# Optimization experiments

Hardware: AMD Instinct MI355X
Metric: run time of the kernel (lower is better)

Reference implementation:

```python
import jax, jax.numpy as jnp
import numpy as np

DILS = [2 ** i for i in range(9)] * 7  # 27 residual-only layers + 36 layers with skip
N0 = 27  # first 27 layers (dilations0) do not contribute to skip connections


def _dconv(x, w, b, d):
    # dilated 'same' conv1d: x [B,C,T], w [O,I,3]
    y = jax.lax.conv_general_dilated(x, w, (1,), [(d, d)], rhs_dilation=(d,),
                                     dimension_numbers=('NCH', 'OIH', 'NCH'))
    return y + b[None, :, None]


def _pw(x, w, b):
    # 1x1 conv: w [O,C], x [B,C,T]
    return jnp.einsum('oc,bct->bot', w, x) + b[None, :, None]


def setup_inputs() -> dict:
    key = jax.random.key(0)
    ks = jax.random.split(key, 13)
    B, T, rd, sd, qd, L = 8, 16384, 128, 128, 256, 63
    s = 0.05
    f = lambda k, sh: jax.random.normal(k, sh, jnp.float32) * s
    return {
        'x': jax.random.normal(ks[0], (B, 1, T), jnp.float32),
        'causal_w': f(ks[1], (rd, 1, 25)),
        'causal_b': f(ks[2], (rd,)),
        'dcnn_w': f(ks[3], (L, rd, rd, 3)),
        'dcnn_b': f(ks[4], (L, rd)),
        'dense_w': f(ks[5], (L, rd, rd)),
        'dense_b': f(ks[6], (L, rd)),
        'skip_w': f(ks[7], (L, sd, rd)),
        'skip_b': f(ks[8], (L, sd)),
        'post1_w': f(ks[9], (sd, sd)),
        'post1_b': f(ks[10], (sd,)),
        'post2_w': f(ks[11], (qd, sd)),
        'post2_b': f(ks[12], (qd,)),
    }


def reference(x, causal_w, causal_b, dcnn_w, dcnn_b, dense_w, dense_b,
              skip_w, skip_b, post1_w, post1_b, post2_w, post2_b):
    # causal conv: kernel 25, padding 12 ('same')
    x = jax.lax.conv_general_dilated(x, causal_w, (1,), [(12, 12)],
                                     dimension_numbers=('NCH', 'OIH', 'NCH'))
    x = x + causal_b[None, :, None]
    B, _, T = x.shape
    skip = jnp.zeros((B, skip_w.shape[1], T), x.dtype)
    for cnt, d in enumerate(DILS):
        xin = x
        h = jax.nn.relu(x)
        h = jax.nn.relu(_dconv(h, dcnn_w[cnt], dcnn_b[cnt], d))
        if cnt >= N0:
            skip = skip + _pw(h, skip_w[cnt], skip_b[cnt])
        x = _pw(h, dense_w[cnt], dense_b[cnt]) + xin
    h = jax.nn.relu(_pw(jax.nn.relu(skip), post1_w, post1_b))
    return _pw(h, post2_w, post2_b)
```

## Files before the change

### kernel.cpp

```cpp
#include <hip/hip_runtime.h>

#define RD     128
#define TT     128
#define TLEN   16384
#define NB     8
#define NLAYER 63
#define N0SKIP 27
#define QD     256
#define PADR   136
#define SROWS  192

typedef short bf16x8 __attribute__((ext_vector_type(8)));
typedef float f32x4  __attribute__((ext_vector_type(4)));

__device__ __forceinline__ unsigned short f2bf(float f) {
  unsigned u = __float_as_uint(f);
  u += 0x7fffu + ((u >> 16) & 1u);
  return (unsigned short)(u >> 16);
}
__device__ __forceinline__ short f2bf_relu(float f) {
  f = f > 0.f ? f : 0.f;
  unsigned u = __float_as_uint(f);
  u += 0x7fffu + ((u >> 16) & 1u);
  return (short)(u >> 16);
}

__device__ __forceinline__ void mfma_gemm(const unsigned short* __restrict__ aw,
                                          const short* sx, int rowbase,
                                          int c0w, int t0w, int n, int q,
                                          f32x4 (&acc)[4][4]) {
#pragma unroll
  for (int ks = 0; ks < 4; ++ks) {
    const int i0 = ks * 32 + q * 8;
    bf16x8 a[4], bb[4];
#pragma unroll
    for (int ct = 0; ct < 4; ++ct)
      a[ct] = *(const bf16x8*)&aw[(size_t)(c0w + ct * 16 + n) * RD + i0];
#pragma unroll
    for (int tt = 0; tt < 4; ++tt)
      bb[tt] = *(const bf16x8*)&sx[(rowbase + t0w + tt * 16 + n) * PADR + i0];
#pragma unroll
    for (int ct = 0; ct < 4; ++ct)
#pragma unroll
      for (int tt = 0; tt < 4; ++tt)
        acc[ct][tt] = __builtin_amdgcn_mfma_f32_16x16x32_bf16(a[ct], bb[tt],
                                                              acc[ct][tt], 0, 0, 0);
  }
}

__device__ __forceinline__ void zero_acc(f32x4 (&acc)[4][4]) {
#pragma unroll
  for (int i = 0; i < 4; ++i)
#pragma unroll
    for (int j = 0; j < 4; ++j) acc[i][j] = (f32x4){0.f, 0.f, 0.f, 0.f};
}

#define SUNROLL 8
__device__ __forceinline__ void stage_rows(short* sx, int rowbase,
                                           const float* __restrict__ xb,
                                           int tstart, int nrows, int tid) {
  const int total = nrows * 32;
  int idx = tid;
  for (; idx + 256 * (SUNROLL - 1) < total; idx += 256 * SUNROLL) {
    float4 v[SUNROLL];
#pragma unroll
    for (int u = 0; u < SUNROLL; ++u) {
      const int i2 = idx + u * 256;
      const int tg = tstart + (i2 >> 5);
      const int c4 = (i2 & 31) << 2;
      v[u] = make_float4(0.f, 0.f, 0.f, 0.f);
      if ((unsigned)tg < (unsigned)TLEN)
        v[u] = *(const float4*)&xb[(size_t)tg * RD + c4];
    }
#pragma unroll
    for (int u = 0; u < SUNROLL; ++u) {
      const int i2 = idx + u * 256;
      const int r = i2 >> 5;
      const int c4 = (i2 & 31) << 2;
      short4 o;
      o.x = f2bf_relu(v[u].x); o.y = f2bf_relu(v[u].y);
      o.z = f2bf_relu(v[u].z); o.w = f2bf_relu(v[u].w);
      *(short4*)&sx[(rowbase + r) * PADR + c4] = o;
    }
  }
  for (; idx < total; idx += 256) {
    const int tg = tstart + (idx >> 5);
    const int c4 = (idx & 31) << 2;
    float4 v = make_float4(0.f, 0.f, 0.f, 0.f);
    if ((unsigned)tg < (unsigned)TLEN)
      v = *(const float4*)&xb[(size_t)tg * RD + c4];
    short4 o;
    o.x = f2bf_relu(v.x); o.y = f2bf_relu(v.y);
    o.z = f2bf_relu(v.z); o.w = f2bf_relu(v.w);
    *(short4*)&sx[(rowbase + (idx >> 5)) * PADR + c4] = o;
  }
}

__device__ __forceinline__ void store_act_bf16(short* dst, const f32x4 (&acc)[4][4],
                                               const float* __restrict__ bias,
                                               int c0w, int t0w, int n, int q) {
#pragma unroll
  for (int ct = 0; ct < 4; ++ct) {
    const int c = c0w + ct * 16 + q * 4;
    const float4 bb = *(const float4*)&bias[c];
#pragma unroll
    for (int tt = 0; tt < 4; ++tt) {
      const int t = t0w + tt * 16 + n;
      const f32x4 A = acc[ct][tt];
      short4 o;
      o.x = f2bf_relu(A[0] + bb.x);
      o.y = f2bf_relu(A[1] + bb.y);
      o.z = f2bf_relu(A[2] + bb.z);
      o.w = f2bf_relu(A[3] + bb.w);
      *(short4*)&dst[t * PADR + c] = o;
    }
  }
}

__device__ __forceinline__ void epi_accum(float* __restrict__ dst,
                                          const float* __restrict__ src,
                                          const float* __restrict__ bias,
                                          const f32x4 (&acc)[4][4],
                                          int c0w, int t0w, int n, int q) {
#pragma unroll
  for (int ct = 0; ct < 4; ++ct) {
    const int c = c0w + ct * 16 + q * 4;
    const float4 bb = *(const float4*)&bias[c];
#pragma unroll
    for (int tt = 0; tt < 4; ++tt) {
      const int t = t0w + tt * 16 + n;
      float4 r = *(const float4*)&src[(size_t)t * RD + c];
      const f32x4 A = acc[ct][tt];
      r.x += A[0] + bb.x; r.y += A[1] + bb.y;
      r.z += A[2] + bb.z; r.w += A[3] + bb.w;
      *(float4*)&dst[(size_t)t * RD + c] = r;
    }
  }
}

__global__ __launch_bounds__(256, 2) void layer_kernel(
    const float* __restrict__ x_in, float* __restrict__ x_out,
    float* __restrict__ skip,
    const unsigned short* __restrict__ wconv,
    const float* __restrict__ bconv,
    const unsigned short* __restrict__ wdense, const float* __restrict__ bdense,
    const unsigned short* __restrict__ wskip,  const float* __restrict__ bskip,
    int dil, int do_skip) {
  __shared__ short sx[SROWS * PADR];

  const int tid = threadIdx.x;
  const int bid = blockIdx.x;
  const int swz = (bid & 7) * 128 + (bid >> 3);
  const int b   = swz >> 7;
  const int t0  = (swz & 127) << 7;
  const int lane = tid & 63;
  const int n = lane & 15, q = lane >> 4;
  const int w = tid >> 6;
  const int c0w = (w & 1) * 64, t0w = (w >> 1) * 64;
  const float* xb = x_in + (size_t)b * TLEN * RD;

  f32x4 acc[4][4];
  zero_acc(acc);

  if (dil <= 32) {
    stage_rows(sx, 0, xb, t0 - dil, 128 + 2 * dil, tid);
    __syncthreads();
    for (int k = 0; k < 3; ++k)
      mfma_gemm(wconv + (size_t)k * RD * RD, sx, k * dil, c0w, t0w, n, q, acc);
  } else if (dil == 64) {
    stage_rows(sx, 0, xb, t0 - 64, 192, tid);
    __syncthreads();
    mfma_gemm(wconv, sx, 0, c0w, t0w, n, q, acc);
    mfma_gemm(wconv + (size_t)RD * RD, sx, 64, c0w, t0w, n, q, acc);
    __syncthreads();
    stage_rows(sx, 0, xb, t0 + 128, 64, tid);
    __syncthreads();
    mfma_gemm(wconv + (size_t)2 * RD * RD, sx, (t0w == 0) ? 128 : -64,
              c0w, t0w, n, q, acc);
  } else {
#pragma unroll
    for (int k = 0; k < 3; ++k) {
      stage_rows(sx, 0, xb, t0 + (k - 1) * dil, 128, tid);
      __syncthreads();
      mfma_gemm(wconv + (size_t)k * RD * RD, sx, 0, c0w, t0w, n, q, acc);
      __syncthreads();
    }
  }
  __syncthreads();

  store_act_bf16(sx, acc, bconv, c0w, t0w, n, q);
  __syncthreads();

  zero_acc(acc);
  mfma_gemm(wdense, sx, 0, c0w, t0w, n, q, acc);
  {
    float* xo = x_out + ((size_t)b * TLEN + t0) * RD;
    const float* xi = x_in + ((size_t)b * TLEN + t0) * RD;
    epi_accum(xo, xi, bdense, acc, c0w, t0w, n, q);
  }

  if (do_skip) {
    zero_acc(acc);
    mfma_gemm(wskip, sx, 0, c0w, t0w, n, q, acc);
    float* sp = skip + ((size_t)b * TLEN + t0) * RD;
    epi_accum(sp, sp, bskip, acc, c0w, t0w, n, q);
  }
}

__global__ __launch_bounds__(256) void causal_kernel(const float* __restrict__ x,
                                                     const float* __restrict__ w,
                                                     const float* __restrict__ bias,
                                                     float* __restrict__ y) {
  __shared__ float xw[152];
  __shared__ float wl[RD * 25];
  __shared__ float bl[RD];
  const int tid = threadIdx.x;
  const int b   = blockIdx.x >> 7;
  const int t0  = (blockIdx.x & 127) << 7;
  for (int i = tid; i < RD * 25; i += 256) wl[i] = w[i];
  if (tid < RD) bl[tid] = bias[tid];
  for (int i = tid; i < 152; i += 256) {
    const int tg = t0 - 12 + i;
    xw[i] = ((unsigned)tg < (unsigned)TLEN) ? x[(size_t)b * TLEN + tg] : 0.f;
  }
  __syncthreads();
  const int c = tid & 127, tp = tid >> 7;
  float* yb = y + ((size_t)b * TLEN + t0) * RD + c;
  const float bc = bl[c];
  for (int i = 0; i < 64; ++i) {
    const int tl = i * 2 + tp;
    float s = bc;
#pragma unroll
    for (int k = 0; k < 25; ++k) s = fmaf(wl[c * 25 + k], xw[tl + k], s);
    yb[(size_t)tl * RD] = s;
  }
}

__global__ __launch_bounds__(256, 1) void post_kernel(
    const float* __restrict__ skip,
    const unsigned short* __restrict__ p1, const float* __restrict__ p1b,
    const unsigned short* __restrict__ p2, const float* __restrict__ p2b,
    float* __restrict__ out) {
  __shared__ short sb[128 * PADR];
  __shared__ short h1[128 * PADR];
  __shared__ float ost[128 * 132];

  const int tid = threadIdx.x;
  const int b   = blockIdx.x >> 7;
  const int t0  = (blockIdx.x & 127) << 7;
  const int lane = tid & 63;
  const int n = lane & 15, q = lane >> 4;
  const int w = tid >> 6;
  const int c0w = (w & 1) * 64, t0w = (w >> 1) * 64;
  const float* skb = skip + ((size_t)b * TLEN + t0) * RD;

  for (int idx = tid; idx < 128 * 32; idx += 256) {
    const int r = idx >> 5, c4 = (idx & 31) << 2;
    float4 v = *(const float4*)&skb[(size_t)r * RD + c4];
    short4 o;
    o.x = f2bf_relu(v.x); o.y = f2bf_relu(v.y);
    o.z = f2bf_relu(v.z); o.w = f2bf_relu(v.w);
    *(short4*)&sb[r * PADR + c4] = o;
  }
  __syncthreads();

  f32x4 acc[4][4];
  zero_acc(acc);
  mfma_gemm(p1, sb, 0, c0w, t0w, n, q, acc);
  store_act_bf16(h1, acc, p1b, c0w, t0w, n, q);
  __syncthreads();

  for (int half = 0; half < 2; ++half) {
    zero_acc(acc);
    mfma_gemm(p2 + (size_t)half * RD * RD, h1, 0, c0w, t0w, n, q, acc);
#pragma unroll
    for (int ct = 0; ct < 4; ++ct) {
      const int c = c0w + ct * 16 + q * 4;
      const float4 bb = *(const float4*)&p2b[half * RD + c];
#pragma unroll
      for (int tt = 0; tt < 4; ++tt) {
        const int t = t0w + tt * 16 + n;
        const f32x4 A = acc[ct][tt];
        ost[(c + 0) * 132 + t] = A[0] + bb.x;
        ost[(c + 1) * 132 + t] = A[1] + bb.y;
        ost[(c + 2) * 132 + t] = A[2] + bb.z;
        ost[(c + 3) * 132 + t] = A[3] + bb.w;
      }
    }
    __syncthreads();
    float* ob = out + ((size_t)b * QD + half * RD) * TLEN + t0;
    for (int idx = tid; idx < 128 * 32; idx += 256) {
      const int r = idx >> 5, t4 = (idx & 31) << 2;
      const float4 v = *(const float4*)&ost[r * 132 + t4];
      *(float4*)&ob[(size_t)r * TLEN + t4] = v;
    }
    __syncthreads();
  }
}

__global__ __launch_bounds__(256) void cvt_kernel(const float* __restrict__ in,
                                                  unsigned short* __restrict__ out,
                                                  int total) {
  const int i = blockIdx.x * 256 + threadIdx.x;
  if (i < total) out[i] = f2bf(in[i]);
}
__global__ __launch_bounds__(256) void cvt_conv_kernel(const float* __restrict__ in,
                                                       unsigned short* __restrict__ out,
                                                       int total) {
  const int idx = blockIdx.x * 256 + threadIdx.x;
  if (idx >= total) return;
  const int ci = idx & 127, co = (idx >> 7) & 127, lk = idx >> 14;
  const int k = lk % 3, l = lk / 3;
  out[idx] = f2bf(in[(((size_t)l * RD + co) * RD + ci) * 3 + k]);
}

extern "C" void kernel_launch(void* const* d_in, const int* in_sizes, int n_in,
                              void* d_out, int out_size, void* d_ws, size_t ws_size,
                              hipStream_t stream) {
  const float* x        = (const float*)d_in[0];
  const float* causal_w = (const float*)d_in[1];
  const float* causal_b = (const float*)d_in[2];
  const float* dcnn_w   = (const float*)d_in[3];
  const float* dcnn_b   = (const float*)d_in[4];
  const float* dense_w  = (const float*)d_in[5];
  const float* dense_b  = (const float*)d_in[6];
  const float* skip_w   = (const float*)d_in[7];
  const float* skip_b   = (const float*)d_in[8];
  const float* post1_w  = (const float*)d_in[9];
  const float* post1_b  = (const float*)d_in[10];
  const float* post2_w  = (const float*)d_in[11];
  const float* post2_b  = (const float*)d_in[12];
  float* out = (float*)d_out;

  const size_t XN = (size_t)NB * TLEN * RD;
  float* ws  = (float*)d_ws;
  float* xA  = ws;
  float* xB  = xA + XN;
  float* skp = xB + XN;
  unsigned short* wc  = (unsigned short*)(skp + XN);
  unsigned short* wd  = wc  + (size_t)NLAYER * 3 * RD * RD;
  unsigned short* wsk = wd  + (size_t)NLAYER * RD * RD;
  unsigned short* p1  = wsk + (size_t)NLAYER * RD * RD;
  unsigned short* p2  = p1  + RD * RD;

  const int tconv = NLAYER * 3 * RD * RD;
  const int t2    = NLAYER * RD * RD;
  cvt_conv_kernel<<<(tconv + 255) / 256, 256, 0, stream>>>(dcnn_w, wc, tconv);
  cvt_kernel<<<(t2 + 255) / 256, 256, 0, stream>>>(dense_w, wd, t2);
  cvt_kernel<<<(t2 + 255) / 256, 256, 0, stream>>>(skip_w, wsk, t2);
  cvt_kernel<<<(RD * RD + 255) / 256, 256, 0, stream>>>(post1_w, p1, RD * RD);
  cvt_kernel<<<(QD * RD + 255) / 256, 256, 0, stream>>>(post2_w, p2, QD * RD);

  causal_kernel<<<NB * (TLEN / TT), 256, 0, stream>>>(x, causal_w, causal_b, xA);
  hipMemsetAsync(skp, 0, XN * sizeof(float), stream);

  const float* src = xA;
  float* dst = xB;
  for (int l = 0; l < NLAYER; ++l) {
    const int dil = 1 << (l % 9);
    layer_kernel<<<NB * (TLEN / TT), 256, 0, stream>>>(
        src, dst, skp,
        wc  + (size_t)l * 3 * RD * RD, dcnn_b  + (size_t)l * RD,
        wd  + (size_t)l * RD * RD,     dense_b + (size_t)l * RD,
        wsk + (size_t)l * RD * RD,     skip_b  + (size_t)l * RD,
        dil, (l >= N0SKIP) ? 1 : 0);
    const float* tmp = src; src = dst; dst = (float*)tmp;
  }

  post_kernel<<<NB * (TLEN / TT), 256, 0, stream>>>(skp, p1, post1_b, p2, post2_b, out);
}
```

Before: 4.824 ms.

## Stage halo reads from a bf16 relu shadow copy and keep residual in place

Each layer now writes, alongside the fp32 residual, a bf16 copy of relu(x), and the next layer stages its dilated-conv input (including halo rows) from that half-size buffer instead of re-reading and converting fp32. The fp32 residual is updated in place in one buffer, and the residual and skip tiles are prefetched into registers before the GEMMs so their loads overlap compute. This trades an extra bf16 store per layer for halving the staging read traffic. It also raises register pressure with two 4x4 float4 tiles held per thread, under a launch bound of two blocks.

```diff
diff --git a/kernel.cpp b/kernel.cpp
--- a/kernel.cpp
+++ b/kernel.cpp
@@ -57,42 +57,32 @@
 
 #define SUNROLL 8
 __device__ __forceinline__ void stage_rows(short* sx, int rowbase,
-                                           const float* __restrict__ xb,
+                                           const unsigned short* __restrict__ shb,
                                            int tstart, int nrows, int tid) {
-  const int total = nrows * 32;
+  const int total = nrows * 16;
   int idx = tid;
   for (; idx + 256 * (SUNROLL - 1) < total; idx += 256 * SUNROLL) {
-    float4 v[SUNROLL];
+    bf16x8 v[SUNROLL];
 #pragma unroll
     for (int u = 0; u < SUNROLL; ++u) {
       const int i2 = idx + u * 256;
-      const int tg = tstart + (i2 >> 5);
-      const int c4 = (i2 & 31) << 2;
-      v[u] = make_float4(0.f, 0.f, 0.f, 0.f);
+      const int tg = tstart + (i2 >> 4);
+      v[u] = (bf16x8)(short)0;
       if ((unsigned)tg < (unsigned)TLEN)
-        v[u] = *(const float4*)&xb[(size_t)tg * RD + c4];
+        v[u] = *(const bf16x8*)&shb[(size_t)tg * RD + ((i2 & 15) << 3)];
     }
 #pragma unroll
     for (int u = 0; u < SUNROLL; ++u) {
       const int i2 = idx + u * 256;
-      const int r = i2 >> 5;
-      const int c4 = (i2 & 31) << 2;
-      short4 o;
-      o.x = f2bf_relu(v[u].x); o.y = f2bf_relu(v[u].y);
-      o.z = f2bf_relu(v[u].z); o.w = f2bf_relu(v[u].w);
-      *(short4*)&sx[(rowbase + r) * PADR + c4] = o;
+      *(bf16x8*)&sx[(rowbase + (i2 >> 4)) * PADR + ((i2 & 15) << 3)] = v[u];
     }
   }
   for (; idx < total; idx += 256) {
-    const int tg = tstart + (idx >> 5);
-    const int c4 = (idx & 31) << 2;
-    float4 v = make_float4(0.f, 0.f, 0.f, 0.f);
+    const int tg = tstart + (idx >> 4);
+    bf16x8 v = (bf16x8)(short)0;
     if ((unsigned)tg < (unsigned)TLEN)
-      v = *(const float4*)&xb[(size_t)tg * RD + c4];
-    short4 o;
-    o.x = f2bf_relu(v.x); o.y = f2bf_relu(v.y);
-    o.z = f2bf_relu(v.z); o.w = f2bf_relu(v.w);
-    *(short4*)&sx[(rowbase + (idx >> 5)) * PADR + c4] = o;
+      v = *(const bf16x8*)&shb[(size_t)tg * RD + ((idx & 15) << 3)];
+    *(bf16x8*)&sx[(rowbase + (idx >> 4)) * PADR + ((idx & 15) << 3)] = v;
   }
 }
 
@@ -117,8 +107,20 @@
   }
 }
 
-__device__ __forceinline__ void epi_accum(float* __restrict__ dst,
-                                          const float* __restrict__ src,
+__device__ __forceinline__ void prefetch_tile(float4 (&r)[4][4],
+                                              const float* __restrict__ src,
+                                              int c0w, int t0w, int n, int q) {
+#pragma unroll
+  for (int ct = 0; ct < 4; ++ct)
+#pragma unroll
+    for (int tt = 0; tt < 4; ++tt)
+      r[ct][tt] = *(const float4*)&src[(size_t)(t0w + tt * 16 + n) * RD +
+                                       c0w + ct * 16 + q * 4];
+}
+
+__device__ __forceinline__ void epi_dense(float* __restrict__ xo,
+                                          unsigned short* __restrict__ so,
+                                          const float4 (&xi)[4][4],
                                           const float* __restrict__ bias,
                                           const f32x4 (&acc)[4][4],
                                           int c0w, int t0w, int n, int q) {
@@ -129,7 +131,32 @@
 #pragma unroll
     for (int tt = 0; tt < 4; ++tt) {
       const int t = t0w + tt * 16 + n;
-      float4 r = *(const float4*)&src[(size_t)t * RD + c];
+      float4 r = xi[ct][tt];
+      const f32x4 A = acc[ct][tt];
+      r.x += A[0] + bb.x; r.y += A[1] + bb.y;
+      r.z += A[2] + bb.z; r.w += A[3] + bb.w;
+      *(float4*)&xo[(size_t)t * RD + c] = r;
+      short4 o;
+      o.x = f2bf_relu(r.x); o.y = f2bf_relu(r.y);
+      o.z = f2bf_relu(r.z); o.w = f2bf_relu(r.w);
+      *(short4*)&so[(size_t)t * RD + c] = o;
+    }
+  }
+}
+
+__device__ __forceinline__ void epi_accum_reg(float* __restrict__ dst,
+                                              const float4 (&src)[4][4],
+                                              const float* __restrict__ bias,
+                                              const f32x4 (&acc)[4][4],
+                                              int c0w, int t0w, int n, int q) {
+#pragma unroll
+  for (int ct = 0; ct < 4; ++ct) {
+    const int c = c0w + ct * 16 + q * 4;
+    const float4 bb = *(const float4*)&bias[c];
+#pragma unroll
+    for (int tt = 0; tt < 4; ++tt) {
+      const int t = t0w + tt * 16 + n;
+      float4 r = src[ct][tt];
       const f32x4 A = acc[ct][tt];
       r.x += A[0] + bb.x; r.y += A[1] + bb.y;
       r.z += A[2] + bb.z; r.w += A[3] + bb.w;
@@ -139,7 +166,9 @@
 }
 
 __global__ __launch_bounds__(256, 2) void layer_kernel(
-    const float* __restrict__ x_in, float* __restrict__ x_out,
+    float* __restrict__ x,
+    const unsigned short* __restrict__ sh_in,
+    unsigned short* __restrict__ sh_out,
     float* __restrict__ skip,
     const unsigned short* __restrict__ wconv,
     const float* __restrict__ bconv,
@@ -157,30 +186,34 @@
   const int n = lane & 15, q = lane >> 4;
   const int w = tid >> 6;
   const int c0w = (w & 1) * 64, t0w = (w >> 1) * 64;
-  const float* xb = x_in + (size_t)b * TLEN * RD;
+  const unsigned short* shb = sh_in + (size_t)b * TLEN * RD;
+  float* xt = x + ((size_t)b * TLEN + t0) * RD;
+
+  float4 xi_r[4][4];
+  prefetch_tile(xi_r, xt, c0w, t0w, n, q);
 
   f32x4 acc[4][4];
   zero_acc(acc);
 
   if (dil <= 32) {
-    stage_rows(sx, 0, xb, t0 - dil, 128 + 2 * dil, tid);
+    stage_rows(sx, 0, shb, t0 - dil, 128 + 2 * dil, tid);
     __syncthreads();
     for (int k = 0; k < 3; ++k)
       mfma_gemm(wconv + (size_t)k * RD * RD, sx, k * dil, c0w, t0w, n, q, acc);
   } else if (dil == 64) {
-    stage_rows(sx, 0, xb, t0 - 64, 192, tid);
+    stage_rows(sx, 0, shb, t0 - 64, 192, tid);
     __syncthreads();
     mfma_gemm(wconv, sx, 0, c0w, t0w, n, q, acc);
     mfma_gemm(wconv + (size_t)RD * RD, sx, 64, c0w, t0w, n, q, acc);
     __syncthreads();
-    stage_rows(sx, 0, xb, t0 + 128, 64, tid);
+    stage_rows(sx, 0, shb, t0 + 128, 64, tid);
     __syncthreads();
     mfma_gemm(wconv + (size_t)2 * RD * RD, sx, (t0w == 0) ? 128 : -64,
               c0w, t0w, n, q, acc);
   } else {
 #pragma unroll
     for (int k = 0; k < 3; ++k) {
-      stage_rows(sx, 0, xb, t0 + (k - 1) * dil, 128, tid);
+      stage_rows(sx, 0, shb, t0 + (k - 1) * dil, 128, tid);
       __syncthreads();
       mfma_gemm(wconv + (size_t)k * RD * RD, sx, 0, c0w, t0w, n, q, acc);
       __syncthreads();
@@ -193,24 +226,24 @@
 
   zero_acc(acc);
   mfma_gemm(wdense, sx, 0, c0w, t0w, n, q, acc);
-  {
-    float* xo = x_out + ((size_t)b * TLEN + t0) * RD;
-    const float* xi = x_in + ((size_t)b * TLEN + t0) * RD;
-    epi_accum(xo, xi, bdense, acc, c0w, t0w, n, q);
-  }
+  epi_dense(xt, sh_out + ((size_t)b * TLEN + t0) * RD, xi_r, bdense, acc,
+            c0w, t0w, n, q);
 
   if (do_skip) {
+    float* sp = skip + ((size_t)b * TLEN + t0) * RD;
+    float4 sk_r[4][4];
+    prefetch_tile(sk_r, sp, c0w, t0w, n, q);
     zero_acc(acc);
     mfma_gemm(wskip, sx, 0, c0w, t0w, n, q, acc);
-    float* sp = skip + ((size_t)b * TLEN + t0) * RD;
-    epi_accum(sp, sp, bskip, acc, c0w, t0w, n, q);
+    epi_accum_reg(sp, sk_r, bskip, acc, c0w, t0w, n, q);
   }
 }
 
 __global__ __launch_bounds__(256) void causal_kernel(const float* __restrict__ x,
                                                      const float* __restrict__ w,
                                                      const float* __restrict__ bias,
-                                                     float* __restrict__ y) {
+                                                     float* __restrict__ y,
+                                                     unsigned short* __restrict__ sh) {
   __shared__ float xw[152];
   __shared__ float wl[RD * 25];
   __shared__ float bl[RD];
@@ -226,6 +259,7 @@
   __syncthreads();
   const int c = tid & 127, tp = tid >> 7;
   float* yb = y + ((size_t)b * TLEN + t0) * RD + c;
+  unsigned short* sb_ = sh + ((size_t)b * TLEN + t0) * RD + c;
   const float bc = bl[c];
   for (int i = 0; i < 64; ++i) {
     const int tl = i * 2 + tp;
@@ -233,6 +267,7 @@
 #pragma unroll
     for (int k = 0; k < 25; ++k) s = fmaf(wl[c * 25 + k], xw[tl + k], s);
     yb[(size_t)tl * RD] = s;
+    sb_[(size_t)tl * RD] = (unsigned short)f2bf_relu(s);
   }
 }
 
@@ -333,11 +368,11 @@
   float* out = (float*)d_out;
 
   const size_t XN = (size_t)NB * TLEN * RD;
-  float* ws  = (float*)d_ws;
-  float* xA  = ws;
-  float* xB  = xA + XN;
-  float* skp = xB + XN;
-  unsigned short* wc  = (unsigned short*)(skp + XN);
+  float* xF  = (float*)d_ws;
+  float* skp = xF + XN;
+  unsigned short* sA  = (unsigned short*)(skp + XN);
+  unsigned short* sB  = sA + XN;
+  unsigned short* wc  = sB + XN;
   unsigned short* wd  = wc  + (size_t)NLAYER * 3 * RD * RD;
   unsigned short* wsk = wd  + (size_t)NLAYER * RD * RD;
   unsigned short* p1  = wsk + (size_t)NLAYER * RD * RD;
@@ -351,20 +386,20 @@
   cvt_kernel<<<(RD * RD + 255) / 256, 256, 0, stream>>>(post1_w, p1, RD * RD);
   cvt_kernel<<<(QD * RD + 255) / 256, 256, 0, stream>>>(post2_w, p2, QD * RD);
 
-  causal_kernel<<<NB * (TLEN / TT), 256, 0, stream>>>(x, causal_w, causal_b, xA);
+  causal_kernel<<<NB * (TLEN / TT), 256, 0, stream>>>(x, causal_w, causal_b, xF, sA);
   hipMemsetAsync(skp, 0, XN * sizeof(float), stream);
 
-  const float* src = xA;
-  float* dst = xB;
+  const unsigned short* ssrc = sA;
+  unsigned short* sdst = sB;
   for (int l = 0; l < NLAYER; ++l) {
     const int dil = 1 << (l % 9);
     layer_kernel<<<NB * (TLEN / TT), 256, 0, stream>>>(
-        src, dst, skp,
+        xF, ssrc, sdst, skp,
         wc  + (size_t)l * 3 * RD * RD, dcnn_b  + (size_t)l * RD,
         wd  + (size_t)l * RD * RD,     dense_b + (size_t)l * RD,
         wsk + (size_t)l * RD * RD,     skip_b  + (size_t)l * RD,
         dil, (l >= N0SKIP) ? 1 : 0);
-    const float* tmp = src; src = dst; dst = (float*)tmp;
+    const unsigned short* tmp = ssrc; ssrc = sdst; sdst = (unsigned short*)tmp;
   }
 
   post_kernel<<<NB * (TLEN / TT), 256, 0, stream>>>(skp, p1, post1_b, p2, post2_b, out);
```

Result: slower. 7.018 ms (+45.5%).
